# Kernel tuning notes

Hardware: AMD Instinct MI355X
Metric: run time of the kernel (lower is better)

The kernel has to match this reference:

```python
import jax, jax.numpy as jnp
import numpy as np

D_MODEL = 1024
N_HEADS = 16
HEAD_DIM = D_MODEL // N_HEADS


def setup_inputs() -> dict:
    key = jax.random.key(0)
    ks = jax.random.split(key, 5)
    B, S = 2, 2048
    x = jax.random.normal(ks[0], (B, S, D_MODEL), dtype=jnp.float32)
    # nn.Linear weights: [out_features, in_features]
    s_in = 1.0 / np.sqrt(D_MODEL)
    qkv_w = jax.random.uniform(ks[1], (3 * D_MODEL, D_MODEL), jnp.float32, -s_in, s_in)
    qkv_b = jax.random.uniform(ks[2], (3 * D_MODEL,), jnp.float32, -s_in, s_in)
    out_w = jax.random.uniform(ks[3], (D_MODEL, D_MODEL), jnp.float32, -s_in, s_in)
    out_b = jax.random.uniform(ks[4], (D_MODEL,), jnp.float32, -s_in, s_in)
    return {"x": x, "qkv_w": qkv_w, "qkv_b": qkv_b, "out_w": out_w, "out_b": out_b}


def reference(x, qkv_w, qkv_b, out_w, out_b):
    B, S, D = x.shape
    H, Hd = N_HEADS, HEAD_DIM
    scale = 1.0 / np.sqrt(Hd)
    qkv = jnp.einsum('bsd,ed->bse', x, qkv_w) + qkv_b  # [B,S,3D]
    qkv = qkv.reshape(B, S, 3, H, Hd)
    q = qkv[:, :, 0].transpose(0, 2, 1, 3)  # [B,H,S,Hd]
    k = qkv[:, :, 1].transpose(0, 2, 1, 3)
    v = qkv[:, :, 2].transpose(0, 2, 1, 3)
    scores = jnp.einsum('bhqd,bhkd->bhqk', q, k) * scale  # [B,H,S,S]
    causal = jnp.triu(jnp.ones((S, S), dtype=bool), k=1)
    scores = jnp.where(causal[None, None], -jnp.inf, scores)
    probs = jax.nn.softmax(scores, axis=-1)
    out = jnp.einsum('bhqk,bhkd->bhqd', probs, v)  # [B,H,S,Hd]
    out = out.transpose(0, 2, 1, 3).reshape(B, S, D)
    out = jnp.einsum('bsd,ed->bse', out, out_w) + out_b
    return out
```

## Files before the change

kernel.cpp:

```cpp
#include <hip/hip_runtime.h>
#include <hip/hip_bf16.h>

#define SEQ    2048
#define DMODEL 1024
#define NHEAD  16
#define HDIM   64
#define BATCH  2
#define NTOK   (BATCH * SEQ)

#define N_X   (NTOK * DMODEL)
#define N_WQ  (3 * DMODEL * DMODEL)
#define N_BQ  (3 * DMODEL)
#define N_WO  (DMODEL * DMODEL)
#define N_BO  (DMODEL)
#define N_CANON (N_X + N_WQ + N_BQ + N_WO + N_BO)

#define NEG_SENT (-1.0e30f)
#define QSCALE 0.1803368801111f

typedef __attribute__((ext_vector_type(8))) short short8;
typedef __attribute__((ext_vector_type(4))) short short4v;
typedef __attribute__((ext_vector_type(4))) float f32x4;
typedef __attribute__((ext_vector_type(16))) float f32x16;

#define MFMA_BF16(A, B, C) __builtin_amdgcn_mfma_f32_16x16x32_bf16((A), (B), (C), 0, 0, 0)
#define MFMA32_BF16(A, B, C) __builtin_amdgcn_mfma_f32_32x32x16_bf16((A), (B), (C), 0, 0, 0)

static __device__ __forceinline__ short8 load8(const __hip_bfloat16* p) {
    return *(const short8*)p;
}

static __device__ __forceinline__ unsigned cvtpk_bf16(float lo, float hi) {
    unsigned r;
    asm("v_cvt_pk_bf16_f32 %0, %1, %2" : "=v"(r) : "v"(lo), "v"(hi));
    return r;
}

static __device__ __forceinline__ void async16(const void* g, void* l) {
    __builtin_amdgcn_global_load_lds(
        (const __attribute__((address_space(1))) unsigned int*)g,
        (__attribute__((address_space(3))) unsigned int*)l,
        16, 0, 0);
}

__global__ __launch_bounds__(256) void canon_kernel(
    const void* __restrict__ s0, const void* __restrict__ s1,
    const void* __restrict__ s2, const void* __restrict__ s3,
    const void* __restrict__ s4,
    __hip_bfloat16* __restrict__ dst, int* __restrict__ flag)
{
    __shared__ int sflag;
    {
        const unsigned short* w = (const unsigned short*)s1;
        if (threadIdx.x < 64) {
            int cnt = 0;
            for (int i = threadIdx.x; i < 512; i += 64) {
                const unsigned e = (w[i] >> 7) & 0xFF;
                if (e >= 125) cnt++;
            }
#pragma unroll
            for (int o = 32; o; o >>= 1) cnt += __shfl_down(cnt, o);
            if (threadIdx.x == 0) sflag = (cnt > 8) ? 1 : 0;
        }
        __syncthreads();
    }
    const int isf32 = sflag;
    if (blockIdx.x == 0 && threadIdx.x == 0) *flag = isf32;

    const int v = blockIdx.x * 256 + threadIdx.x;
    if (v >= N_CANON / 8) return;
    const int idx = v * 8;
    const void* src;
    int off;
    if (idx < N_X)                          { src = s0; off = idx; }
    else if (idx < N_X + N_WQ)              { src = s1; off = idx - N_X; }
    else if (idx < N_X + N_WQ + N_BQ)       { src = s2; off = idx - (N_X + N_WQ); }
    else if (idx < N_X + N_WQ + N_BQ + N_WO){ src = s3; off = idx - (N_X + N_WQ + N_BQ); }
    else                                    { src = s4; off = idx - (N_X + N_WQ + N_BQ + N_WO); }
    if (isf32) {
        const f32x4* sp = (const f32x4*)((const float*)src + off);
        const f32x4 x0 = sp[0], x1 = sp[1];
        short8 o;
#pragma unroll
        for (int j = 0; j < 4; ++j) {
            o[j]     = (short)__bfloat16_as_ushort(__float2bfloat16(x0[j]));
            o[4 + j] = (short)__bfloat16_as_ushort(__float2bfloat16(x1[j]));
        }
        *(short8*)&dst[idx] = o;
    } else {
        *(short8*)&dst[idx] = *(const short8*)((const __hip_bfloat16*)src + off);
    }
}

__global__ __launch_bounds__(256) void qkv_gemm_kernel(
    const __hip_bfloat16* __restrict__ X,
    const __hip_bfloat16* __restrict__ W,
    const __hip_bfloat16* __restrict__ bias,
    __hip_bfloat16* __restrict__ Qs,
    __hip_bfloat16* __restrict__ Kb,
    __hip_bfloat16* __restrict__ Vt)
{
    constexpr int Kd = DMODEL;
    __shared__ __align__(16) __hip_bfloat16 As[3][128 * 32];
    __shared__ __align__(16) __hip_bfloat16 Bs[3][128 * 32];

    const int tid   = threadIdx.x;
    const int lane  = tid & 63;
    const int w     = tid >> 6;
    const int mTile = blockIdx.y * 128;
    const int nTile = blockIdx.x * 128;
    const int wm    = (w >> 1) * 64;
    const int wn    = (w & 1) * 64;
    const int lm    = lane & 15;
    const int q4    = lane >> 4;
    const int lks   = (q4 ^ ((lm >> 1) & 3)) * 8;

    f32x4 acc[4][4];
#pragma unroll
    for (int i = 0; i < 4; ++i)
#pragma unroll
        for (int j = 0; j < 4; ++j)
            acc[i][j] = (f32x4){0.f, 0.f, 0.f, 0.f};

    const int r0c = tid >> 2;
    const int r1c = (tid + 256) >> 2;
    const int cbs = ((tid & 3) ^ ((tid >> 3) & 3)) * 8;

    const __hip_bfloat16* gA0 = &X[(size_t)(mTile + r0c) * Kd + cbs];
    const __hip_bfloat16* gA1 = &X[(size_t)(mTile + r1c) * Kd + cbs];
    const __hip_bfloat16* gB0 = &W[(size_t)(nTile + r0c) * Kd + cbs];
    const __hip_bfloat16* gB1 = &W[(size_t)(nTile + r1c) * Kd + cbs];

    async16(gA0, (char*)As[0] + tid * 16);
    async16(gA1, (char*)As[0] + tid * 16 + 4096);
    async16(gB0, (char*)Bs[0] + tid * 16);
    async16(gB1, (char*)Bs[0] + tid * 16 + 4096);
    async16(gA0 + 32, (char*)As[1] + tid * 16);
    async16(gA1 + 32, (char*)As[1] + tid * 16 + 4096);
    async16(gB0 + 32, (char*)Bs[1] + tid * 16);
    async16(gB1 + 32, (char*)Bs[1] + tid * 16 + 4096);

    int cur = 0;
    constexpr int NIT = Kd / 32;
    for (int it = 0; it < NIT; ++it) {
        if (it + 1 < NIT) {
            asm volatile("s_waitcnt vmcnt(4)" ::: "memory");
        } else {
            asm volatile("s_waitcnt vmcnt(0)" ::: "memory");
        }
        __builtin_amdgcn_s_barrier();
        __builtin_amdgcn_sched_barrier(0);

        if (it + 2 < NIT) {
            const int slot = (cur + 2 >= 3) ? cur - 1 : cur + 2;
            const int k2 = (it + 2) * 32;
            async16(gA0 + k2, (char*)As[slot] + tid * 16);
            async16(gA1 + k2, (char*)As[slot] + tid * 16 + 4096);
            async16(gB0 + k2, (char*)Bs[slot] + tid * 16);
            async16(gB1 + k2, (char*)Bs[slot] + tid * 16 + 4096);
        }

        const __hip_bfloat16* Ac = As[cur];
        const __hip_bfloat16* Bc = Bs[cur];
        short8 a[4], b[4];
#pragma unroll
        for (int i = 0; i < 4; ++i)
            a[i] = *(const short8*)&Ac[(wm + i * 16 + lm) * 32 + lks];
#pragma unroll
        for (int j = 0; j < 4; ++j)
            b[j] = *(const short8*)&Bc[(wn + j * 16 + lm) * 32 + lks];
#pragma unroll
        for (int i = 0; i < 4; ++i)
#pragma unroll
            for (int j = 0; j < 4; ++j)
                acc[i][j] = MFMA_BF16(a[i], b[j], acc[i][j]);

        cur = (cur + 1 == 3) ? 0 : cur + 1;
    }

    const int r0 = (lane >> 4) * 4;
#pragma unroll
    for (int j = 0; j < 4; ++j) {
        const int n  = nTile + wn + j * 16 + lm;
        const float bv = __bfloat162float(bias[n]);
        const int c = n >> 10;
        const int h = (n >> 6) & 15;
        const int d = n & 63;
#pragma unroll
        for (int i = 0; i < 4; ++i) {
            if (c == 2) {
                const int m0 = mTile + wm + i * 16 + r0;
                const int bb = m0 >> 11;
                const int s0 = m0 & (SEQ - 1);
                const int bh = bb * NHEAD + h;
                short4v pk;
#pragma unroll
                for (int r = 0; r < 4; ++r)
                    pk[r] = (short)__bfloat16_as_ushort(
                        __float2bfloat16(acc[i][j][r] + bv));
                *(short4v*)&Vt[(size_t)(bh * HDIM + d) * SEQ + s0] = pk;
            } else {
#pragma unroll
                for (int r = 0; r < 4; ++r) {
                    const int m  = mTile + wm + i * 16 + r0 + r;
                    const int bb = m >> 11;
                    const int s  = m & (SEQ - 1);
                    const int bh = bb * NHEAD + h;
                    const float v = acc[i][j][r] + bv;
                    if (c == 0) {
                        Qs[(size_t)(bh * SEQ + s) * HDIM + d] = __float2bfloat16(v * QSCALE);
                    } else {
                        Kb[(size_t)(bh * SEQ + s) * HDIM + d] = __float2bfloat16(v);
                    }
                }
            }
        }
    }
}

__global__ __launch_bounds__(256, 3) void attn_kernel(
    const __hip_bfloat16* __restrict__ Qs,
    const __hip_bfloat16* __restrict__ Kb,
    const __hip_bfloat16* __restrict__ Vt,
    float* __restrict__ Opart,
    float* __restrict__ MLpart)
{
    __shared__ __align__(16) __hip_bfloat16 Kt[2][64 * 64];
    __shared__ __align__(16) __hip_bfloat16 Vs[2][64 * 64];

    const int tid  = threadIdx.x;
    const int lane = tid & 63;
    const int wv   = tid >> 6;
    const int bh   = blockIdx.x;
    const int py   = blockIdx.y;
    const int p    = py / 3;
    const int j3   = py % 3;

    const int c_lo = (j3 == 0) ? 0 : (j3 == 1 ? 12 : 23);
    const int c_hi = (j3 == 0) ? 12 : (j3 == 1 ? 23 : 34);
    const int bnd  = 32 - 2 * p;

    const int lq = lane & 31;
    const int sg = lane >> 5;
    const int swr = lq & 7;

    const __hip_bfloat16* Qbh = Qs + (size_t)bh * SEQ * HDIM;
    const __hip_bfloat16* Kbh = Kb + (size_t)bh * SEQ * HDIM;
    const __hip_bfloat16* Vbh = Vt + (size_t)bh * HDIM * SEQ;

    const int srow0 = tid >> 3;
    const int scb   = (tid & 7) ^ (srow0 & 7);

    for (int seg = 0; seg < 2; ++seg) {
        int qb, a, b, slot;
        if (seg == 0) {
            if (j3 == 2 && p >= 5) continue;
            qb = 15 - p; a = c_lo;
            b  = (c_hi < bnd) ? c_hi : bnd;
            slot = j3;
        } else {
            if (j3 == 0 || (j3 == 1 && p <= 4)) continue;
            qb = p;
            a  = ((c_lo > bnd) ? c_lo : bnd) - bnd;
            b  = c_hi - bnd;
            slot = (j3 == 2) ? 3 : 4;
        }

        const int wbase = qb * 128 + wv * 32;
        const int qrow  = wbase + lq;

        short8 qa[4];
#pragma unroll
        for (int s = 0; s < 4; ++s)
            qa[s] = load8(&Qbh[(size_t)qrow * HDIM + s * 16 + sg * 8]);

        float m_run = NEG_SENT;
        float l_run = 0.f;
        f32x16 Oacc[2];
#pragma unroll
        for (int t = 0; t < 2; ++t)
#pragma unroll
            for (int e = 0; e < 16; ++e) Oacc[t][e] = 0.f;

        __builtin_amdgcn_s_barrier();

        {
            const int kk0 = a * 64;
            async16(&Kbh[(size_t)(kk0 + srow0) * HDIM + scb * 8],      (char*)Kt[0] + tid * 16);
            async16(&Kbh[(size_t)(kk0 + srow0 + 32) * HDIM + scb * 8], (char*)Kt[0] + tid * 16 + 4096);
            async16(&Vbh[(size_t)srow0 * SEQ + kk0 + scb * 8],         (char*)Vs[0] + tid * 16);
            async16(&Vbh[(size_t)(srow0 + 32) * SEQ + kk0 + scb * 8],  (char*)Vs[0] + tid * 16 + 4096);
            if (a + 1 < b) {
                const int kk1 = kk0 + 64;
                async16(&Kbh[(size_t)(kk1 + srow0) * HDIM + scb * 8],      (char*)Kt[1] + tid * 16);
                async16(&Kbh[(size_t)(kk1 + srow0 + 32) * HDIM + scb * 8], (char*)Kt[1] + tid * 16 + 4096);
                async16(&Vbh[(size_t)srow0 * SEQ + kk1 + scb * 8],         (char*)Vs[1] + tid * 16);
                async16(&Vbh[(size_t)(srow0 + 32) * SEQ + kk1 + scb * 8],  (char*)Vs[1] + tid * 16 + 4096);
            }
        }

        int cur = 0;
        for (int ci = a; ci < b; ++ci) {
            const int k0 = ci * 64;

            if (ci + 1 < b) {
                asm volatile("s_waitcnt vmcnt(4)" ::: "memory");
            } else {
                asm volatile("s_waitcnt vmcnt(0)" ::: "memory");
            }
            __builtin_amdgcn_s_barrier();
            __builtin_amdgcn_sched_barrier(0);

            if (k0 <= wbase + 31) {
                const __hip_bfloat16* Kc = Kt[cur];
                const __hip_bfloat16* Vc = Vs[cur];

                f32x16 sc[2];
#pragma unroll
                for (int t = 0; t < 2; ++t)
#pragma unroll
                    for (int e = 0; e < 16; ++e) sc[t][e] = 0.f;
#pragma unroll
                for (int t = 0; t < 2; ++t)
#pragma unroll
                    for (int s = 0; s < 4; ++s) {
                        const short8 ka = *(const short8*)&Kc[
                            (t * 32 + lq) * 64 + (((s * 2 + sg) ^ swr) * 8)];
                        sc[t] = MFMA32_BF16(ka, qa[s], sc[t]);
                    }

                if (k0 + 63 > wbase) {
#pragma unroll
                    for (int t = 0; t < 2; ++t)
#pragma unroll
                        for (int g = 0; g < 4; ++g)
#pragma unroll
                            for (int r = 0; r < 4; ++r) {
                                const int key = k0 + t * 32 + r + 8 * g + 4 * sg;
                                if (key > qrow) sc[t][g * 4 + r] = NEG_SENT;
                            }
                }

                float mx = sc[0][0];
#pragma unroll
                for (int t = 0; t < 2; ++t)
#pragma unroll
                    for (int e = 0; e < 16; ++e) mx = fmaxf(mx, sc[t][e]);
                mx = fmaxf(mx, __shfl_xor(mx, 32));

                if (!__all(mx <= m_run + 8.0f)) {
                    const float mn = fmaxf(m_run, mx);
                    const float alpha = exp2f(m_run - mn);
                    m_run = mn;
                    l_run *= alpha;
#pragma unroll
                    for (int t = 0; t < 2; ++t)
#pragma unroll
                        for (int e = 0; e < 16; ++e) Oacc[t][e] *= alpha;
                }

                float ssum = 0.f;
#pragma unroll
                for (int t = 0; t < 2; ++t)
#pragma unroll
                    for (int e = 0; e < 16; ++e) {
                        const float pv = exp2f(sc[t][e] - m_run);
                        sc[t][e] = pv;
                        ssum += pv;
                    }
                ssum += __shfl_xor(ssum, 32);
                l_run += ssum;

                unsigned wpk[2][4][2];
#pragma unroll
                for (int t = 0; t < 2; ++t)
#pragma unroll
                    for (int g = 0; g < 4; ++g) {
                        wpk[t][g][0] = cvtpk_bf16(sc[t][g * 4 + 0], sc[t][g * 4 + 1]);
                        wpk[t][g][1] = cvtpk_bf16(sc[t][g * 4 + 2], sc[t][g * 4 + 3]);
                    }

#pragma unroll
                for (int s = 0; s < 4; ++s) {
                    const int t  = s >> 1;
                    const int gp = (s & 1) * 2;
                    const unsigned oe0 = wpk[t][gp][0],     oe1 = wpk[t][gp][1];
                    const unsigned oo0 = wpk[t][gp + 1][0], oo1 = wpk[t][gp + 1][1];
                    const unsigned pay0 = sg ? oe0 : oo0;
                    const unsigned pay1 = sg ? oe1 : oo1;
                    const unsigned rc0 = (unsigned)__shfl_xor((int)pay0, 32);
                    const unsigned rc1 = (unsigned)__shfl_xor((int)pay1, 32);
                    unsigned f[4];
                    f[0] = sg ? rc0 : oe0;
                    f[1] = sg ? rc1 : oe1;
                    f[2] = sg ? oo0 : rc0;
                    f[3] = sg ? oo1 : rc1;
                    const short8 pa = *(const short8*)f;
#pragma unroll
                    for (int t2 = 0; t2 < 2; ++t2) {
                        const short8 va = *(const short8*)&Vc[
                            (t2 * 32 + lq) * 64 + (((s * 2 + sg) ^ swr) * 8)];
                        Oacc[t2] = MFMA32_BF16(va, pa, Oacc[t2]);
                    }
                }
            }

            __builtin_amdgcn_s_barrier();
            if (ci + 2 < b) {
                const int kk = (ci + 2) * 64;
                async16(&Kbh[(size_t)(kk + srow0) * HDIM + scb * 8],      (char*)Kt[cur] + tid * 16);
                async16(&Kbh[(size_t)(kk + srow0 + 32) * HDIM + scb * 8], (char*)Kt[cur] + tid * 16 + 4096);
                async16(&Vbh[(size_t)srow0 * SEQ + kk + scb * 8],         (char*)Vs[cur] + tid * 16);
                async16(&Vbh[(size_t)(srow0 + 32) * SEQ + kk + scb * 8],  (char*)Vs[cur] + tid * 16 + 4096);
            }
            cur ^= 1;
        }

        const size_t pbase = ((size_t)(bh * 8 + p) * 5 + slot) * 128;
        const size_t orow  = (pbase + wv * 32 + lq) * 64;
#pragma unroll
        for (int t2 = 0; t2 < 2; ++t2)
#pragma unroll
            for (int g = 0; g < 4; ++g) {
                f32x4 v;
#pragma unroll
                for (int r = 0; r < 4; ++r) v[r] = Oacc[t2][g * 4 + r];
                *(f32x4*)&Opart[orow + t2 * 32 + 8 * g + 4 * sg] = v;
            }
        if (lane < 32) {
            MLpart[(pbase + wv * 32 + lane) * 2 + 0] = m_run;
            MLpart[(pbase + wv * 32 + lane) * 2 + 1] = l_run;
        }
    }
}

__global__ __launch_bounds__(256) void attn_merge_kernel(
    const float* __restrict__ Opart, const float* __restrict__ MLpart,
    __hip_bfloat16* __restrict__ O)
{
    const int idx  = blockIdx.x * 256 + threadIdx.x;
    const int d16  = idx & 3;
    const int grow = idx >> 2;
    const int bh   = grow >> 11;
    const int s    = grow & 2047;
    const int qb   = s >> 7;
    const int rin  = s & 127;

    const bool heavy = (qb >= 8);
    const int p  = heavy ? (15 - qb) : qb;
    const int s0 = heavy ? 0 : 3;
    const int s1 = heavy ? 1 : 4;
    const bool v1 = heavy ? true : (p >= 5);
    const bool v2 = heavy && (p <= 4);

    const size_t rb = (size_t)(bh * 8 + p) * 5;
    const size_t r0 = (rb + s0) * 128 + rin;
    const size_t r1 = (rb + s1) * 128 + rin;
    const size_t r2 = (rb + 2)  * 128 + rin;

    const float m0 = MLpart[r0 * 2],                 l0 = MLpart[r0 * 2 + 1];
    const float m1 = v1 ? MLpart[r1 * 2] : NEG_SENT, l1 = v1 ? MLpart[r1 * 2 + 1] : 0.f;
    const float m2 = v2 ? MLpart[r2 * 2] : NEG_SENT, l2 = v2 ? MLpart[r2 * 2 + 1] : 0.f;

    float mm = fmaxf(m0, fmaxf(m1, m2));
    const float a0 = exp2f(m0 - mm);
    const float a1 = v1 ? exp2f(m1 - mm) : 0.f;
    const float a2 = v2 ? exp2f(m2 - mm) : 0.f;
    const float inv = 1.0f / (a0 * l0 + a1 * l1 + a2 * l2);

    f32x4 o[4];
    {
        const f32x4* O0 = (const f32x4*)&Opart[r0 * 64 + d16 * 16];
#pragma unroll
        for (int v = 0; v < 4; ++v) o[v] = a0 * O0[v];
    }
    if (v1) {
        const f32x4* O1 = (const f32x4*)&Opart[r1 * 64 + d16 * 16];
#pragma unroll
        for (int v = 0; v < 4; ++v) o[v] += a1 * O1[v];
    }
    if (v2) {
        const f32x4* O2 = (const f32x4*)&Opart[r2 * 64 + d16 * 16];
#pragma unroll
        for (int v = 0; v < 4; ++v) o[v] += a2 * O2[v];
    }

    short8 out[2];
#pragma unroll
    for (int v = 0; v < 4; ++v)
#pragma unroll
        for (int jj = 0; jj < 4; ++jj)
            out[v >> 1][(v & 1) * 4 + jj] = (short)__bfloat16_as_ushort(
                __float2bfloat16(o[v][jj] * inv));

    const int b = bh >> 4, hh = bh & 15;
    __hip_bfloat16* dst = &O[((size_t)b * SEQ + s) * DMODEL + hh * 64 + d16 * 16];
    ((short8*)dst)[0] = out[0];
    ((short8*)dst)[1] = out[1];
}

__global__ __launch_bounds__(256) void proj_gemm_kernel(
    const __hip_bfloat16* __restrict__ A,
    const __hip_bfloat16* __restrict__ W,
    const __hip_bfloat16* __restrict__ bias,
    void* __restrict__ outv,
    const int* __restrict__ flag)
{
    constexpr int Kd = DMODEL;
    __shared__ __align__(16) __hip_bfloat16 As[3][128 * 32];
    __shared__ __align__(16) __hip_bfloat16 Bs[3][64 * 32];

    const int tid   = threadIdx.x;
    const int lane  = tid & 63;
    const int w     = tid >> 6;
    const int mTile = blockIdx.y * 128;
    const int nTile = blockIdx.x * 64;
    const int wm    = (w >> 1) * 64;
    const int wn    = (w & 1) * 32;
    const int lm    = lane & 15;
    const int q4    = lane >> 4;
    const int lks   = (q4 ^ ((lm >> 1) & 3)) * 8;
    const bool f32out = (*flag != 0);

    f32x4 acc[4][2];
#pragma unroll
    for (int i = 0; i < 4; ++i)
#pragma unroll
        for (int j = 0; j < 2; ++j)
            acc[i][j] = (f32x4){0.f, 0.f, 0.f, 0.f};

    const int r0c = tid >> 2;
    const int r1c = (tid + 256) >> 2;
    const int cbs = ((tid & 3) ^ ((tid >> 3) & 3)) * 8;

    const __hip_bfloat16* gA0 = &A[(size_t)(mTile + r0c) * Kd + cbs];
    const __hip_bfloat16* gA1 = &A[(size_t)(mTile + r1c) * Kd + cbs];
    const __hip_bfloat16* gB0 = &W[(size_t)(nTile + r0c) * Kd + cbs];

    async16(gA0, (char*)As[0] + tid * 16);
    async16(gA1, (char*)As[0] + tid * 16 + 4096);
    async16(gB0, (char*)Bs[0] + tid * 16);
    async16(gA0 + 32, (char*)As[1] + tid * 16);
    async16(gA1 + 32, (char*)As[1] + tid * 16 + 4096);
    async16(gB0 + 32, (char*)Bs[1] + tid * 16);

    int cur = 0;
    constexpr int NIT = Kd / 32;
    for (int it = 0; it < NIT; ++it) {
        if (it + 1 < NIT) {
            asm volatile("s_waitcnt vmcnt(3)" ::: "memory");
        } else {
            asm volatile("s_waitcnt vmcnt(0)" ::: "memory");
        }
        __builtin_amdgcn_s_barrier();
        __builtin_amdgcn_sched_barrier(0);

        if (it + 2 < NIT) {
            const int slot = (cur + 2 >= 3) ? cur - 1 : cur + 2;
            const int k2 = (it + 2) * 32;
            async16(gA0 + k2, (char*)As[slot] + tid * 16);
            async16(gA1 + k2, (char*)As[slot] + tid * 16 + 4096);
            async16(gB0 + k2, (char*)Bs[slot] + tid * 16);
        }

        const __hip_bfloat16* Ac = As[cur];
        const __hip_bfloat16* Bc = Bs[cur];
        short8 a[4], b[2];
#pragma unroll
        for (int i = 0; i < 4; ++i)
            a[i] = *(const short8*)&Ac[(wm + i * 16 + lm) * 32 + lks];
#pragma unroll
        for (int j = 0; j < 2; ++j)
            b[j] = *(const short8*)&Bc[(wn + j * 16 + lm) * 32 + lks];
#pragma unroll
        for (int i = 0; i < 4; ++i)
#pragma unroll
            for (int j = 0; j < 2; ++j)
                acc[i][j] = MFMA_BF16(a[i], b[j], acc[i][j]);

        cur = (cur + 1 == 3) ? 0 : cur + 1;
    }

    const int r0 = (lane >> 4) * 4;
#pragma unroll
    for (int j = 0; j < 2; ++j) {
        const int n = nTile + wn + j * 16 + lm;
        const float bv = __bfloat162float(bias[n]);
#pragma unroll
        for (int i = 0; i < 4; ++i) {
#pragma unroll
            for (int r = 0; r < 4; ++r) {
                const size_t m = mTile + wm + i * 16 + r0 + r;
                const float v = acc[i][j][r] + bv;
                if (f32out) ((float*)outv)[m * DMODEL + n] = v;
                else ((__hip_bfloat16*)outv)[m * DMODEL + n] = __float2bfloat16(v);
            }
        }
    }
}

extern "C" void kernel_launch(void* const* d_in, const int* in_sizes, int n_in,
                              void* d_out, int out_size, void* d_ws, size_t ws_size,
                              hipStream_t stream) {
    const size_t OFF_CANON = 256;
    const size_t OFF_QS = OFF_CANON + (size_t)N_CANON * 2;
    const size_t OFF_KB = OFF_QS + (size_t)NTOK * DMODEL * 2;
    const size_t OFF_VT = OFF_KB + (size_t)NTOK * DMODEL * 2;
    const size_t OFF_AO = OFF_VT + (size_t)NTOK * DMODEL * 2;
    const size_t OFF_OP = OFF_AO + (size_t)NTOK * DMODEL * 2;
    const size_t OFF_ML = OFF_OP + (size_t)32 * 8 * 5 * 128 * 64 * 4;

    char* wsb = (char*)d_ws;
    int* flag = (int*)wsb;
    __hip_bfloat16* canon = (__hip_bfloat16*)(wsb + OFF_CANON);
    __hip_bfloat16* Xc = canon;
    __hip_bfloat16* Wq = Xc + N_X;
    __hip_bfloat16* Bq = Wq + N_WQ;
    __hip_bfloat16* Wo = Bq + N_BQ;
    __hip_bfloat16* Bo = Wo + N_WO;
    __hip_bfloat16* Qs = (__hip_bfloat16*)(wsb + OFF_QS);
    __hip_bfloat16* Kb = (__hip_bfloat16*)(wsb + OFF_KB);
    __hip_bfloat16* Vt = (__hip_bfloat16*)(wsb + OFF_VT);
    __hip_bfloat16* Ao = (__hip_bfloat16*)(wsb + OFF_AO);
    float* Opart = (float*)(wsb + OFF_OP);
    float* MLpart = (float*)(wsb + OFF_ML);

    canon_kernel<<<(N_CANON / 8 + 255) / 256, 256, 0, stream>>>(
        d_in[0], d_in[1], d_in[2], d_in[3], d_in[4], canon, flag);

    {
        dim3 grid(3 * DMODEL / 128, NTOK / 128);
        qkv_gemm_kernel<<<grid, 256, 0, stream>>>(Xc, Wq, Bq, Qs, Kb, Vt);
    }
    {
        dim3 grid(BATCH * NHEAD, 24);
        attn_kernel<<<grid, 256, 0, stream>>>(Qs, Kb, Vt, Opart, MLpart);
        attn_merge_kernel<<<(NTOK * NHEAD * 4) / 256, 256, 0, stream>>>(
            Opart, MLpart, Ao);
    }
    {
        dim3 grid(DMODEL / 64, NTOK / 128);
        proj_gemm_kernel<<<grid, 256, 0, stream>>>(Ao, Wo, Bo, d_out, flag);
    }
}
```

Baseline: 192.6 us.

## Split paired causal attention work four ways instead of three

Changes the split-K partitioning of paired heavy/light query blocks from three chunks to four, raising the attention grid from 24 to 32 blocks per head and adding a sixth partial slot. The merge kernel now combines up to four partials per row. The attention kernel's launch bounds are raised to request four blocks per CU. This gives more parallelism and better CU fill, in exchange for more partial-output traffic, more merge work, and tighter register limits.

```diff
diff --git a/kernel.cpp b/kernel.cpp
--- a/kernel.cpp
+++ b/kernel.cpp
@@ -218,7 +218,7 @@
     }
 }
 
-__global__ __launch_bounds__(256, 3) void attn_kernel(
+__global__ __launch_bounds__(256, 4) void attn_kernel(
     const __hip_bfloat16* __restrict__ Qs,
     const __hip_bfloat16* __restrict__ Kb,
     const __hip_bfloat16* __restrict__ Vt,
@@ -233,11 +233,11 @@
     const int wv   = tid >> 6;
     const int bh   = blockIdx.x;
     const int py   = blockIdx.y;
-    const int p    = py / 3;
-    const int j3   = py % 3;
-
-    const int c_lo = (j3 == 0) ? 0 : (j3 == 1 ? 12 : 23);
-    const int c_hi = (j3 == 0) ? 12 : (j3 == 1 ? 23 : 34);
+    const int p    = py >> 2;
+    const int j4   = py & 3;
+
+    const int c_lo = (j4 == 0) ? 0 : (j4 == 1 ? 9 : (j4 == 2 ? 17 : 26));
+    const int c_hi = (j4 == 0) ? 9 : (j4 == 1 ? 17 : (j4 == 2 ? 26 : 34));
     const int bnd  = 32 - 2 * p;
 
     const int lq = lane & 31;
@@ -254,16 +254,16 @@
     for (int seg = 0; seg < 2; ++seg) {
         int qb, a, b, slot;
         if (seg == 0) {
-            if (j3 == 2 && p >= 5) continue;
+            if (c_lo >= bnd) continue;
             qb = 15 - p; a = c_lo;
             b  = (c_hi < bnd) ? c_hi : bnd;
-            slot = j3;
+            slot = j4;
         } else {
-            if (j3 == 0 || (j3 == 1 && p <= 4)) continue;
+            if (c_hi <= bnd) continue;
             qb = p;
             a  = ((c_lo > bnd) ? c_lo : bnd) - bnd;
             b  = c_hi - bnd;
-            slot = (j3 == 2) ? 3 : 4;
+            slot = (j4 == 3) ? ((p <= 3) ? 4 : 5) : 4;
         }
 
         const int wbase = qb * 128 + wv * 32;
@@ -416,7 +416,7 @@
             cur ^= 1;
         }
 
-        const size_t pbase = ((size_t)(bh * 8 + p) * 5 + slot) * 128;
+        const size_t pbase = ((size_t)(bh * 8 + p) * 6 + slot) * 128;
         const size_t orow  = (pbase + wv * 32 + lq) * 64;
 #pragma unroll
         for (int t2 = 0; t2 < 2; ++t2)
@@ -448,41 +448,51 @@
 
     const bool heavy = (qb >= 8);
     const int p  = heavy ? (15 - qb) : qb;
-    const int s0 = heavy ? 0 : 3;
-    const int s1 = heavy ? 1 : 4;
-    const bool v1 = heavy ? true : (p >= 5);
-    const bool v2 = heavy && (p <= 4);
-
-    const size_t rb = (size_t)(bh * 8 + p) * 5;
-    const size_t r0 = (rb + s0) * 128 + rin;
-    const size_t r1 = (rb + s1) * 128 + rin;
-    const size_t r2 = (rb + 2)  * 128 + rin;
-
-    const float m0 = MLpart[r0 * 2],                 l0 = MLpart[r0 * 2 + 1];
-    const float m1 = v1 ? MLpart[r1 * 2] : NEG_SENT, l1 = v1 ? MLpart[r1 * 2 + 1] : 0.f;
-    const float m2 = v2 ? MLpart[r2 * 2] : NEG_SENT, l2 = v2 ? MLpart[r2 * 2 + 1] : 0.f;
-
-    float mm = fmaxf(m0, fmaxf(m1, m2));
-    const float a0 = exp2f(m0 - mm);
-    const float a1 = v1 ? exp2f(m1 - mm) : 0.f;
-    const float a2 = v2 ? exp2f(m2 - mm) : 0.f;
-    const float inv = 1.0f / (a0 * l0 + a1 * l1 + a2 * l2);
+    const size_t rb = (size_t)(bh * 8 + p) * 6;
+
+    const int sA = heavy ? 0 : 4;
+    const int sB = heavy ? 1 : 5;
+    const bool vB = heavy ? true : (p >= 4);
+    const bool vC = heavy;
+    const bool vD = heavy && (p <= 2);
+
+    const size_t rA = (rb + sA) * 128 + rin;
+    const size_t rB = (rb + sB) * 128 + rin;
+    const size_t rC = (rb + 2)  * 128 + rin;
+    const size_t rD = (rb + 3)  * 128 + rin;
+
+    const float mA = MLpart[rA * 2],                 lA = MLpart[rA * 2 + 1];
+    const float mB = vB ? MLpart[rB * 2] : NEG_SENT, lB = vB ? MLpart[rB * 2 + 1] : 0.f;
+    const float mC = vC ? MLpart[rC * 2] : NEG_SENT, lC = vC ? MLpart[rC * 2 + 1] : 0.f;
+    const float mD = vD ? MLpart[rD * 2] : NEG_SENT, lD = vD ? MLpart[rD * 2 + 1] : 0.f;
+
+    const float mm = fmaxf(fmaxf(mA, mB), fmaxf(mC, mD));
+    const float aA = exp2f(mA - mm);
+    const float aB = vB ? exp2f(mB - mm) : 0.f;
+    const float aC = vC ? exp2f(mC - mm) : 0.f;
+    const float aD = vD ? exp2f(mD - mm) : 0.f;
+    const float inv = 1.0f / (aA * lA + aB * lB + aC * lC + aD * lD);
 
     f32x4 o[4];
     {
-        const f32x4* O0 = (const f32x4*)&Opart[r0 * 64 + d16 * 16];
-#pragma unroll
-        for (int v = 0; v < 4; ++v) o[v] = a0 * O0[v];
-    }
-    if (v1) {
-        const f32x4* O1 = (const f32x4*)&Opart[r1 * 64 + d16 * 16];
-#pragma unroll
-        for (int v = 0; v < 4; ++v) o[v] += a1 * O1[v];
-    }
-    if (v2) {
-        const f32x4* O2 = (const f32x4*)&Opart[r2 * 64 + d16 * 16];
-#pragma unroll
-        for (int v = 0; v < 4; ++v) o[v] += a2 * O2[v];
+        const f32x4* OA = (const f32x4*)&Opart[rA * 64 + d16 * 16];
+#pragma unroll
+        for (int v = 0; v < 4; ++v) o[v] = aA * OA[v];
+    }
+    if (vB) {
+        const f32x4* OB = (const f32x4*)&Opart[rB * 64 + d16 * 16];
+#pragma unroll
+        for (int v = 0; v < 4; ++v) o[v] += aB * OB[v];
+    }
+    if (vC) {
+        const f32x4* OC = (const f32x4*)&Opart[rC * 64 + d16 * 16];
+#pragma unroll
+        for (int v = 0; v < 4; ++v) o[v] += aC * OC[v];
+    }
+    if (vD) {
+        const f32x4* OD = (const f32x4*)&Opart[rD * 64 + d16 * 16];
+#pragma unroll
+        for (int v = 0; v < 4; ++v) o[v] += aD * OD[v];
     }
 
     short8 out[2];
@@ -608,7 +618,7 @@
     const size_t OFF_VT = OFF_KB + (size_t)NTOK * DMODEL * 2;
     const size_t OFF_AO = OFF_VT + (size_t)NTOK * DMODEL * 2;
     const size_t OFF_OP = OFF_AO + (size_t)NTOK * DMODEL * 2;
-    const size_t OFF_ML = OFF_OP + (size_t)32 * 8 * 5 * 128 * 64 * 4;
+    const size_t OFF_ML = OFF_OP + (size_t)32 * 8 * 6 * 128 * 64 * 4;
 
     char* wsb = (char*)d_ws;
     int* flag = (int*)wsb;
@@ -633,7 +643,7 @@
         qkv_gemm_kernel<<<grid, 256, 0, stream>>>(Xc, Wq, Bq, Qs, Kb, Vt);
     }
     {
-        dim3 grid(BATCH * NHEAD, 24);
+        dim3 grid(BATCH * NHEAD, 32);
         attn_kernel<<<grid, 256, 0, stream>>>(Qs, Kb, Vt, Opart, MLpart);
         attn_merge_kernel<<<(NTOK * NHEAD * 4) / 256, 256, 0, stream>>>(
             Opart, MLpart, Ao);
```

Measured after the change: 195.9 us. No clear change (+1.7%).
